# Kernel optimization log

Measured on AMD Instinct MI355X. Metric: run time of the kernel, lower is better.

## Reference

```python
import jax, jax.numpy as jnp
import numpy as np

B, H, W = 1, 48, 160
CIN, CF, D = 1024, 64, 48  # input_features, PSM_features, depth_channel = max_disp/downsample
EPS = 1e-5


def setup_inputs() -> dict:
    key = jax.random.key(0)
    ks = jax.random.split(key, 12)
    z = lambda s: jnp.zeros(s, jnp.float32)
    o = lambda s: jnp.ones(s, jnp.float32)
    return {
        "left_features": jax.random.normal(ks[0], (B, CIN, H, W), jnp.float32),
        "right_features": jax.random.normal(ks[1], (B, CIN, H, W), jnp.float32),
        "conv1_w": jax.random.normal(ks[2], (CF, CIN), jnp.float32) * 0.03,
        "conv1_b": z((CF,)),
        "bn1_g": o((CF,)), "bn1_b": z((CF,)),
        "bn1_m": jax.random.normal(ks[3], (CF,), jnp.float32) * 0.1,
        "bn1_v": jax.random.uniform(ks[4], (CF,), jnp.float32) + 0.5,
        "c3a_w": jax.random.normal(ks[5], (CF, 2 * CF, 3, 3, 3), jnp.float32) * 0.02,
        "c3a_b": z((CF,)),
        "bn3a_g": o((CF,)), "bn3a_b": z((CF,)),
        "bn3a_m": jax.random.normal(ks[6], (CF,), jnp.float32) * 0.1,
        "bn3a_v": jax.random.uniform(ks[7], (CF,), jnp.float32) + 0.5,
        "c3b_w": jax.random.normal(ks[8], (CF, CF, 3, 3, 3), jnp.float32) * 0.02,
        "c3b_b": z((CF,)),
        "bn3b_g": o((CF,)), "bn3b_b": z((CF,)),
        "bn3b_m": jax.random.normal(ks[9], (CF,), jnp.float32) * 0.1,
        "bn3b_v": jax.random.uniform(ks[10], (CF,), jnp.float32) + 0.5,
    }


def _bn(x, g, b, m, v, nsp):
    # eval-mode batchnorm; nsp = number of trailing spatial dims
    sh = (-1,) + (1,) * nsp
    return (x - m.reshape(sh)) * (g.reshape(sh) * jax.lax.rsqrt(v.reshape(sh) + EPS)) + b.reshape(sh)


def reference(left_features, right_features, conv1_w, conv1_b, bn1_g, bn1_b, bn1_m, bn1_v,
              c3a_w, c3a_b, bn3a_g, bn3a_b, bn3a_m, bn3a_v,
              c3b_w, c3b_b, bn3b_g, bn3b_b, bn3b_m, bn3b_v):
    def down(x):
        y = jnp.einsum('oi,bihw->bohw', conv1_w, x) + conv1_b[:, None, None]
        return jax.nn.relu(_bn(y, bn1_g, bn1_b, bn1_m, bn1_v, 2))

    L = down(left_features)   # [B,CF,H,W]
    R = down(right_features)  # [B,CF,H,W]

    # Vectorized shifted cost volume (replaces the Python loop over disparities).
    # For disparity d, output width j: left -> L[...,j] if j>=d else 0; right -> R[...,j-d] if j>=d else 0.
    idx = jnp.arange(W)[None, :] - jnp.arange(D)[:, None]       # [D,W]
    mask = (idx >= 0).astype(L.dtype)                           # [D,W]
    left_vol = L[:, :, :, None, :] * mask                       # [B,CF,H,D,W]
    right_vol = R[:, :, :, jnp.clip(idx, 0, W - 1)] * mask      # [B,CF,H,D,W]
    cost = jnp.concatenate([left_vol, right_vol], axis=1)       # [B,2CF,H,D,W]
    cost = jnp.transpose(cost, (0, 1, 3, 2, 4))                 # [B,2CF,D,H,W]

    def conv3(x, wk, bias):
        y = jax.lax.conv_general_dilated(x, wk, (1, 1, 1), [(1, 1)] * 3,
                                         dimension_numbers=('NCDHW', 'OIDHW', 'NCDHW'))
        return y + bias[:, None, None, None]

    y = jax.nn.relu(_bn(conv3(cost, c3a_w, c3a_b), bn3a_g, bn3a_b, bn3a_m, bn3a_v, 3))
    y = jax.nn.relu(_bn(conv3(y, c3b_w, c3b_b), bn3b_g, bn3b_b, bn3b_m, bn3b_v, 3))
    return y.reshape(B, -1, H, W)  # [B, CF*D, H, W]
```

## Files before the change

kernel.cpp:

```cpp
#include <hip/hip_runtime.h>
#include <hip/hip_bf16.h>


#define HH   48
#define WW   160
#define DDEP 48
#define CIN  1024
#define NPX  (HH*WW)
#define KSPL 8

typedef unsigned short u16;
typedef unsigned int   u32;
typedef __attribute__((ext_vector_type(8))) short bf16x8;
typedef __attribute__((ext_vector_type(4))) float f32x4;
typedef __attribute__((ext_vector_type(4))) u32   u32x4;
typedef __attribute__((ext_vector_type(2))) u32   u32x2;

__device__ __forceinline__ u16 f2bf(float f) {
    u32 u = __builtin_bit_cast(u32, f);
    u32 r = u + 0x7FFFu + ((u >> 16) & 1u);
    return (u16)(r >> 16);
}

__global__ __launch_bounds__(256) void k_prep(
    const float* __restrict__ c3a, const float* __restrict__ c3b,
    const float* __restrict__ cb3a, const float* __restrict__ g3a,
    const float* __restrict__ b3a,  const float* __restrict__ m3a,
    const float* __restrict__ v3a,
    const float* __restrict__ cb3b, const float* __restrict__ g3b,
    const float* __restrict__ b3b,  const float* __restrict__ m3b,
    const float* __restrict__ v3b,
    u16* __restrict__ wa, u16* __restrict__ wb, float* __restrict__ bnc)
{
    int tid = blockIdx.x*256 + threadIdx.x;
    if (tid < 221184) {
        int i = tid & 127, o = (tid >> 7) & 63, tap = tid >> 13;
        wa[tid] = f2bf(c3a[(o*128 + i)*27 + tap]);
    } else {
        int t2 = tid - 221184;
        if (t2 < 110592) {
            int i = t2 & 63;
            int kw = (t2 >> 6) % 3;
            int rest = t2 / 192;
            int o = rest & 63, kdkh = rest >> 6;
            wb[t2] = f2bf(c3b[(o*64 + i)*27 + (kdkh/3)*9 + (kdkh%3)*3 + kw]);
        }
    }
    if (tid < 64) {
        float s = g3a[tid] * rsqrtf(v3a[tid] + 1e-5f);
        bnc[tid]      = s;
        bnc[64 + tid] = (cb3a[tid] - m3a[tid])*s + b3a[tid];
    } else if (tid < 128) {
        int o = tid - 64;
        float s = g3b[o] * rsqrtf(v3b[o] + 1e-5f);
        bnc[128 + o] = s;
        bnc[192 + o] = (cb3b[o] - m3b[o])*s + b3b[o];
    }
}

__global__ __launch_bounds__(256) void k_conv1(
    const float* __restrict__ left, const float* __restrict__ right,
    const float* __restrict__ w1, float* __restrict__ P)
{
    const int img = blockIdx.y;
    const int s   = blockIdx.z;
    const float* x = img ? right : left;
    const int px = blockIdx.x*64 + (threadIdx.x & 63);
    const int o0 = (threadIdx.x >> 6)*16;

    float acc[16];
    #pragma unroll
    for (int oo = 0; oo < 16; ++oo) acc[oo] = 0.f;

    const int ibase = s*(CIN/KSPL);
    for (int it = 0; it < CIN/KSPL; it += 4) {
        const int i = ibase + it;
        float x0 = x[(i+0)*NPX + px];
        float x1 = x[(i+1)*NPX + px];
        float x2 = x[(i+2)*NPX + px];
        float x3 = x[(i+3)*NPX + px];
        #pragma unroll
        for (int oo = 0; oo < 16; ++oo) {
            const float4 wv4 = *(const float4*)(w1 + (size_t)(o0+oo)*CIN + i);
            acc[oo] = fmaf(wv4.w, x3, fmaf(wv4.z, x2,
                      fmaf(wv4.y, x1, fmaf(wv4.x, x0, acc[oo]))));
        }
    }
    float* dst = P + ((size_t)(s*2 + img)*NPX + px)*64 + o0;
    #pragma unroll
    for (int q = 0; q < 4; ++q)
        *(f32x4*)(dst + q*4) = *(const f32x4*)(acc + q*4);
}

__global__ __launch_bounds__(256) void k_conv1_reduce(
    const float* __restrict__ P,
    const float* __restrict__ b1,
    const float* __restrict__ g,  const float* __restrict__ bb,
    const float* __restrict__ m,  const float* __restrict__ v,
    u16* __restrict__ LRb)
{
    const int tid = blockIdx.x*256 + threadIdx.x;
    const int f = tid*4;
    f32x4 acc = *(const f32x4*)(P + f);
    #pragma unroll
    for (int s = 1; s < KSPL; ++s)
        acc += *(const f32x4*)(P + (size_t)(s*2)*(NPX*64) + f);
    const int o0 = f & 63;
    u16 res[4];
    #pragma unroll
    for (int r = 0; r < 4; ++r) {
        int o = o0 + r;
        float sc = g[o] * rsqrtf(v[o] + 1e-5f);
        float val = (acc[r] + b1[o] - m[o])*sc + bb[o];
        res[r] = f2bf(val > 0.f ? val : 0.f);
    }
    *(u32x2*)(LRb + f) = *(const u32x2*)res;
}

__global__ __launch_bounds__(256) void k_conv3a(
    const u16* __restrict__ LRb, const u16* __restrict__ wa,
    const float* __restrict__ bnc, u16* __restrict__ yt)
{
    __shared__ u16 sm[31744];
    u16* Lt = sm;
    u16* Rt = sm + 11520;
    u16* Aw = sm + 23040;

    const int h  = blockIdx.x;
    const int d0 = blockIdx.y*2;
    const int tid = threadIdx.x;
    const int l  = tid & 63;
    const int wv = tid >> 6;
    const int dd = wv >> 1;
    const int wbase = (wv & 1)*80;
    const int l15 = l & 15, l4 = l >> 4;
    const int wcol = wbase + l15;
    const bf16x8 bzero = {0,0,0,0,0,0,0,0};

    f32x4 acc[4][5];
    #pragma unroll
    for (int a = 0; a < 4; ++a)
        #pragma unroll
        for (int b = 0; b < 5; ++b)
            acc[a][b] = (f32x4){0.f,0.f,0.f,0.f};

    for (int kh = 0; kh < 3; ++kh) {
        int hp = h + kh - 1;
        if (hp < 0 || hp >= HH) continue;
        __syncthreads();
        {
            const u16* ls = LRb + (size_t)hp*WW*64;
            const u16* rs = LRb + (size_t)(NPX + hp*WW)*64;
            #pragma unroll
            for (int gq = 0; gq < 5; ++gq) {
                int eb = (gq*256 + tid)*8;
                int wwi = eb >> 6, ii = eb & 63;
                u32x4 va = *(const u32x4*)(ls + eb);
                u32x4 vb = *(const u32x4*)(rs + eb);
                *(u32x4*)(Lt + wwi*72 + ii) = va;
                *(u32x4*)(Rt + wwi*72 + ii) = vb;
            }
        }
        for (int kd = 0; kd < 3; ++kd) {
            int dp = d0 + dd + kd - 1;
            bool dok = (dp >= 0) && (dp < DDEP);
            for (int kw = 0; kw < 3; ++kw) {
                __syncthreads();
                {
                    const u16* as = wa + (size_t)(kd*9 + kh*3 + kw)*8192;
                    #pragma unroll
                    for (int gq = 0; gq < 4; ++gq) {
                        int eb = (gq*256 + tid)*8;
                        int o = eb >> 7, ii = eb & 127;
                        *(u32x4*)(Aw + o*136 + ii) = *(const u32x4*)(as + eb);
                    }
                }
                __syncthreads();

                int laddr[5], raddr[5];
                bool val[5];
                #pragma unroll
                for (int nf = 0; nf < 5; ++nf) {
                    int wp = wcol + nf*16 + kw - 1;
                    bool vv = dok && (wp >= 0) && (wp < WW) && (wp >= dp);
                    val[nf]   = vv;
                    laddr[nf] = (vv ? wp : 0)*72;
                    raddr[nf] = (vv ? (wp - dp) : 0)*72;
                }
                #pragma unroll
                for (int ic = 0; ic < 4; ++ic) {
                    const int kcolA = ic*32 + 8*l4;
                    bf16x8 a0 = *(const bf16x8*)(Aw + ( 0 + l15)*136 + kcolA);
                    bf16x8 a1 = *(const bf16x8*)(Aw + (16 + l15)*136 + kcolA);
                    bf16x8 a2 = *(const bf16x8*)(Aw + (32 + l15)*136 + kcolA);
                    bf16x8 a3 = *(const bf16x8*)(Aw + (48 + l15)*136 + kcolA);
                    const int kin = (ic & 1)*32 + 8*l4;
                    #pragma unroll
                    for (int nf = 0; nf < 5; ++nf) {
                        const u16* bp = (ic < 2) ? (Lt + laddr[nf] + kin)
                                                 : (Rt + raddr[nf] + kin);
                        bf16x8 b = *(const bf16x8*)bp;
                        b = val[nf] ? b : bzero;
                        acc[0][nf] = __builtin_amdgcn_mfma_f32_16x16x32_bf16(a0, b, acc[0][nf], 0, 0, 0);
                        acc[1][nf] = __builtin_amdgcn_mfma_f32_16x16x32_bf16(a1, b, acc[1][nf], 0, 0, 0);
                        acc[2][nf] = __builtin_amdgcn_mfma_f32_16x16x32_bf16(a2, b, acc[2][nf], 0, 0, 0);
                        acc[3][nf] = __builtin_amdgcn_mfma_f32_16x16x32_bf16(a3, b, acc[3][nf], 0, 0, 0);
                    }
                }
            }
        }
    }

    __syncthreads();
    u16* eps = sm + wv*5280;
    float sc[4][4], sh[4][4];
    #pragma unroll
    for (int mf = 0; mf < 4; ++mf)
        #pragma unroll
        for (int r = 0; r < 4; ++r) {
            int o = mf*16 + 4*l4 + r;
            sc[mf][r] = bnc[o];
            sh[mf][r] = bnc[64 + o];
        }
    #pragma unroll
    for (int mf = 0; mf < 4; ++mf)
        #pragma unroll
        for (int nf = 0; nf < 5; ++nf)
            #pragma unroll
            for (int r = 0; r < 4; ++r) {
                float vv = acc[mf][nf][r]*sc[mf][r] + sh[mf][r];
                vv = vv > 0.f ? vv : 0.f;
                eps[(nf*16 + l15)*66 + mf*16 + 4*l4 + r] = f2bf(vv);
            }
    const int dy = d0 + dd;
    u16* yb2 = yt + ((size_t)(dy*HH + h)*8)*1280;
    #pragma unroll
    for (int k = 0; k < 40; ++k) {
        int flat = k*64 + l;
        int c   = flat / 320;
        int rem = flat - c*320;
        int w   = rem >> 2;
        int pr  = (rem & 3)*2;
        u32 vv = *(const u32*)(eps + w*66 + c*8 + pr);
        *(u32*)(yb2 + (size_t)c*1280 + (wbase + w)*8 + pr) = vv;
    }
}

__global__ __launch_bounds__(256) void k_conv3b(
    const u16* __restrict__ yt, const u16* __restrict__ wb,
    const float* __restrict__ bnc, float* __restrict__ outp)
{
    __shared__ u16 A2[12800];

    const int h  = blockIdx.x;
    const int d0 = blockIdx.y*2;
    const int tid = threadIdx.x;
    const int l  = tid & 63;
    const int wv = tid >> 6;
    const int dd = wv >> 1;
    const int wbase = (wv & 1)*80;
    const int l15 = l & 15, l4 = l >> 4;
    const int wcol = wbase + l15;
    const bf16x8 bzero = {0,0,0,0,0,0,0,0};

    f32x4 acc[4][5];
    #pragma unroll
    for (int a = 0; a < 4; ++a)
        #pragma unroll
        for (int b = 0; b < 5; ++b)
            acc[a][b] = (f32x4){0.f,0.f,0.f,0.f};

    for (int kh = 0; kh < 3; ++kh) {
        int hp = h + kh - 1;
        if (hp < 0 || hp >= HH) continue;
        for (int kd = 0; kd < 3; ++kd) {
            __syncthreads();
            {
                const u16* as = wb + (size_t)(kd*3 + kh)*12288;
                #pragma unroll
                for (int q = 0; q < 6; ++q) {
                    int idx = q*256 + tid;
                    int o = idx/24;
                    int cc = (idx - o*24)*8;
                    *(u32x4*)(A2 + o*200 + cc) = *(const u32x4*)(as + (size_t)idx*8);
                }
            }
            __syncthreads();

            const int dpw = d0 + dd + kd - 1;
            const bool dok = (dpw >= 0) && (dpw < DDEP);
            const int dc = min(max(dpw, 0), DDEP-1);
            const u16* yrow = yt + ((size_t)((dc*HH + hp)*8) + l4)*1280;
            for (int kw = 0; kw < 3; ++kw) {
                int gofs[5]; bool val[5];
                #pragma unroll
                for (int nf = 0; nf < 5; ++nf) {
                    int wp = wcol + nf*16 + kw - 1;
                    bool vv = dok && (wp >= 0) && (wp < WW);
                    val[nf]  = vv;
                    gofs[nf] = (vv ? wp : 0)*8;
                }
                #pragma unroll
                for (int ic = 0; ic < 2; ++ic) {
                    const int kcolA = kw*64 + ic*32 + 8*l4;
                    bf16x8 a0 = *(const bf16x8*)(A2 + ( 0 + l15)*200 + kcolA);
                    bf16x8 a1 = *(const bf16x8*)(A2 + (16 + l15)*200 + kcolA);
                    bf16x8 a2 = *(const bf16x8*)(A2 + (32 + l15)*200 + kcolA);
                    bf16x8 a3 = *(const bf16x8*)(A2 + (48 + l15)*200 + kcolA);
                    const u16* yc = yrow + ic*5120;
                    #pragma unroll
                    for (int nf = 0; nf < 5; ++nf) {
                        bf16x8 b = *(const bf16x8*)(yc + gofs[nf]);
                        b = val[nf] ? b : bzero;
                        acc[0][nf] = __builtin_amdgcn_mfma_f32_16x16x32_bf16(a0, b, acc[0][nf], 0, 0, 0);
                        acc[1][nf] = __builtin_amdgcn_mfma_f32_16x16x32_bf16(a1, b, acc[1][nf], 0, 0, 0);
                        acc[2][nf] = __builtin_amdgcn_mfma_f32_16x16x32_bf16(a2, b, acc[2][nf], 0, 0, 0);
                        acc[3][nf] = __builtin_amdgcn_mfma_f32_16x16x32_bf16(a3, b, acc[3][nf], 0, 0, 0);
                    }
                }
            }
        }
    }

    const int dout = d0 + dd;
    #pragma unroll
    for (int mf = 0; mf < 4; ++mf)
        #pragma unroll
        for (int r = 0; r < 4; ++r) {
            int o = mf*16 + 4*l4 + r;
            float s = bnc[128 + o], t = bnc[192 + o];
            size_t base = ((size_t)(o*DDEP + dout)*HH + h)*WW + wbase;
            #pragma unroll
            for (int nf = 0; nf < 5; ++nf) {
                float vv = acc[mf][nf][r]*s + t;
                outp[base + nf*16 + l15] = vv > 0.f ? vv : 0.f;
            }
        }
}

extern "C" void kernel_launch(void* const* d_in, const int* in_sizes, int n_in,
                              void* d_out, int out_size, void* d_ws, size_t ws_size,
                              hipStream_t stream)
{
    const float* left  = (const float*)d_in[0];
    const float* right = (const float*)d_in[1];
    const float* w1    = (const float*)d_in[2];
    const float* b1    = (const float*)d_in[3];
    const float* g1    = (const float*)d_in[4];
    const float* bb1   = (const float*)d_in[5];
    const float* m1    = (const float*)d_in[6];
    const float* v1    = (const float*)d_in[7];
    const float* c3a   = (const float*)d_in[8];
    const float* cb3a  = (const float*)d_in[9];
    const float* g3a   = (const float*)d_in[10];
    const float* b3a   = (const float*)d_in[11];
    const float* m3a   = (const float*)d_in[12];
    const float* v3a   = (const float*)d_in[13];
    const float* c3b   = (const float*)d_in[14];
    const float* cb3b  = (const float*)d_in[15];
    const float* g3b   = (const float*)d_in[16];
    const float* b3b   = (const float*)d_in[17];
    const float* m3b   = (const float*)d_in[18];
    const float* v3b   = (const float*)d_in[19];

    char* ws = (char*)d_ws;
    u16*   LRb = (u16*)ws;
    u16*   wa  = (u16*)(ws + 1966080);
    u16*   wb  = (u16*)(ws + 1966080 + 442368);
    float* bnc = (float*)(ws + 1966080 + 442368 + 221184);
    u16*   yt  = (u16*)(ws + 1966080 + 442368 + 221184 + 1024);
    if (ws_size < 49816576) return;

    float* P = (float*)d_out;

    k_prep<<<dim3(1296), dim3(256), 0, stream>>>(
        c3a, c3b, cb3a, g3a, b3a, m3a, v3a, cb3b, g3b, b3b, m3b, v3b, wa, wb, bnc);
    k_conv1<<<dim3(120, 2, KSPL), dim3(256), 0, stream>>>(
        left, right, w1, P);
    k_conv1_reduce<<<dim3(960), dim3(256), 0, stream>>>(
        P, b1, g1, bb1, m1, v1, LRb);
    k_conv3a<<<dim3(48, 24), dim3(256), 0, stream>>>(LRb, wa, bnc, yt);
    k_conv3b<<<dim3(48, 24), dim3(256), 0, stream>>>(yt, wb, bnc, (float*)d_out);
}
```

Measured before the change: 389.7 us.

## Stage conv1 weights in LDS and read conv3a inputs directly in channel-blocked layout

Conv1 now loads its slice of the weight matrix into shared memory once per block, so the inner loop no longer re-reads weights from global memory. The conv1 reduce writes the downsampled features in a channel-blocked [img][h][c/8][w][8] layout. Conv3a then reads its B operands straight from global memory in that layout instead of staging left and right rows through LDS, and writes its outputs directly without the LDS epilogue transpose. This frees LDS and removes barriers, but conv3a now depends on cache hits for repeated global reads, and the stride-1280 pattern may coalesce less well.

After: 358.8 us. -7.9%, faster.

```diff
diff --git a/kernel.cpp b/kernel.cpp
--- a/kernel.cpp
+++ b/kernel.cpp
@@ -62,17 +62,28 @@
     const float* __restrict__ left, const float* __restrict__ right,
     const float* __restrict__ w1, float* __restrict__ P)
 {
+    __shared__ float Ws[8192];
     const int img = blockIdx.y;
     const int s   = blockIdx.z;
     const float* x = img ? right : left;
-    const int px = blockIdx.x*64 + (threadIdx.x & 63);
-    const int o0 = (threadIdx.x >> 6)*16;
+    const int tid = threadIdx.x;
+    const int px = blockIdx.x*64 + (tid & 63);
+    const int o0 = (tid >> 6)*16;
+    const int ibase = s*(CIN/KSPL);
+
+    #pragma unroll
+    for (int q = 0; q < 8; ++q) {
+        int idx = q*256 + tid;
+        int o = idx >> 5, ii = (idx & 31)*4;
+        *(f32x4*)(Ws + o*128 + ii) =
+            *(const f32x4*)(w1 + (size_t)o*CIN + ibase + ii);
+    }
+    __syncthreads();
 
     float acc[16];
     #pragma unroll
     for (int oo = 0; oo < 16; ++oo) acc[oo] = 0.f;
 
-    const int ibase = s*(CIN/KSPL);
     for (int it = 0; it < CIN/KSPL; it += 4) {
         const int i = ibase + it;
         float x0 = x[(i+0)*NPX + px];
@@ -81,7 +92,7 @@
         float x3 = x[(i+3)*NPX + px];
         #pragma unroll
         for (int oo = 0; oo < 16; ++oo) {
-            const float4 wv4 = *(const float4*)(w1 + (size_t)(o0+oo)*CIN + i);
+            const float4 wv4 = *(const float4*)(Ws + (o0+oo)*128 + it);
             acc[oo] = fmaf(wv4.w, x3, fmaf(wv4.z, x2,
                       fmaf(wv4.y, x1, fmaf(wv4.x, x0, acc[oo]))));
         }
@@ -106,6 +117,9 @@
     for (int s = 1; s < KSPL; ++s)
         acc += *(const f32x4*)(P + (size_t)(s*2)*(NPX*64) + f);
     const int o0 = f & 63;
+    const int px = f >> 6;
+    const int img = px / NPX, pxl = px - img*NPX;
+    const int h = pxl / WW, w = pxl - h*WW;
     u16 res[4];
     #pragma unroll
     for (int r = 0; r < 4; ++r) {
@@ -114,17 +128,16 @@
         float val = (acc[r] + b1[o] - m[o])*sc + bb[o];
         res[r] = f2bf(val > 0.f ? val : 0.f);
     }
-    *(u32x2*)(LRb + f) = *(const u32x2*)res;
+    u16* dst = LRb + (size_t)img*491520 + h*10240 + (o0 >> 3)*1280
+                   + w*8 + (o0 & 7);
+    *(u32x2*)dst = *(const u32x2*)res;
 }
 
 __global__ __launch_bounds__(256) void k_conv3a(
     const u16* __restrict__ LRb, const u16* __restrict__ wa,
     const float* __restrict__ bnc, u16* __restrict__ yt)
 {
-    __shared__ u16 sm[31744];
-    u16* Lt = sm;
-    u16* Rt = sm + 11520;
-    u16* Aw = sm + 23040;
+    __shared__ u16 Aw[8704];
 
     const int h  = blockIdx.x;
     const int d0 = blockIdx.y*2;
@@ -147,23 +160,11 @@
     for (int kh = 0; kh < 3; ++kh) {
         int hp = h + kh - 1;
         if (hp < 0 || hp >= HH) continue;
-        __syncthreads();
-        {
-            const u16* ls = LRb + (size_t)hp*WW*64;
-            const u16* rs = LRb + (size_t)(NPX + hp*WW)*64;
-            #pragma unroll
-            for (int gq = 0; gq < 5; ++gq) {
-                int eb = (gq*256 + tid)*8;
-                int wwi = eb >> 6, ii = eb & 63;
-                u32x4 va = *(const u32x4*)(ls + eb);
-                u32x4 vb = *(const u32x4*)(rs + eb);
-                *(u32x4*)(Lt + wwi*72 + ii) = va;
-                *(u32x4*)(Rt + wwi*72 + ii) = vb;
-            }
-        }
+        const u16* lrow = LRb + (size_t)hp*10240;
+        const u16* rrow = LRb + 491520 + (size_t)hp*10240;
         for (int kd = 0; kd < 3; ++kd) {
-            int dp = d0 + dd + kd - 1;
-            bool dok = (dp >= 0) && (dp < DDEP);
+            const int dp = d0 + dd + kd - 1;
+            const bool dok = (dp >= 0) && (dp < DDEP);
             for (int kw = 0; kw < 3; ++kw) {
                 __syncthreads();
                 {
@@ -177,15 +178,15 @@
                 }
                 __syncthreads();
 
-                int laddr[5], raddr[5];
+                int lofs[5], rofs[5];
                 bool val[5];
                 #pragma unroll
                 for (int nf = 0; nf < 5; ++nf) {
                     int wp = wcol + nf*16 + kw - 1;
                     bool vv = dok && (wp >= 0) && (wp < WW) && (wp >= dp);
-                    val[nf]   = vv;
-                    laddr[nf] = (vv ? wp : 0)*72;
-                    raddr[nf] = (vv ? (wp - dp) : 0)*72;
+                    val[nf]  = vv;
+                    lofs[nf] = (vv ? wp : 0)*8;
+                    rofs[nf] = (vv ? (wp - dp) : 0)*8;
                 }
                 #pragma unroll
                 for (int ic = 0; ic < 4; ++ic) {
@@ -194,12 +195,12 @@
                     bf16x8 a1 = *(const bf16x8*)(Aw + (16 + l15)*136 + kcolA);
                     bf16x8 a2 = *(const bf16x8*)(Aw + (32 + l15)*136 + kcolA);
                     bf16x8 a3 = *(const bf16x8*)(Aw + (48 + l15)*136 + kcolA);
-                    const int kin = (ic & 1)*32 + 8*l4;
+                    const u16* bbase = ((ic < 2) ? lrow : rrow)
+                                     + (size_t)((ic & 1)*4 + l4)*1280;
                     #pragma unroll
                     for (int nf = 0; nf < 5; ++nf) {
-                        const u16* bp = (ic < 2) ? (Lt + laddr[nf] + kin)
-                                                 : (Rt + raddr[nf] + kin);
-                        bf16x8 b = *(const bf16x8*)bp;
+                        bf16x8 b = *(const bf16x8*)(bbase +
+                                       ((ic < 2) ? lofs[nf] : rofs[nf]));
                         b = val[nf] ? b : bzero;
                         acc[0][nf] = __builtin_amdgcn_mfma_f32_16x16x32_bf16(a0, b, acc[0][nf], 0, 0, 0);
                         acc[1][nf] = __builtin_amdgcn_mfma_f32_16x16x32_bf16(a1, b, acc[1][nf], 0, 0, 0);
@@ -211,8 +212,6 @@
         }
     }
 
-    __syncthreads();
-    u16* eps = sm + wv*5280;
     float sc[4][4], sh[4][4];
     #pragma unroll
     for (int mf = 0; mf < 4; ++mf)
@@ -222,28 +221,24 @@
             sc[mf][r] = bnc[o];
             sh[mf][r] = bnc[64 + o];
         }
+    const int dy = d0 + dd;
+    u16* rowb = yt + (size_t)(dy*HH + h)*10240;
     #pragma unroll
     for (int mf = 0; mf < 4; ++mf)
         #pragma unroll
-        for (int nf = 0; nf < 5; ++nf)
+        for (int nf = 0; nf < 5; ++nf) {
+            const int w = wbase + nf*16 + l15;
             #pragma unroll
-            for (int r = 0; r < 4; ++r) {
-                float vv = acc[mf][nf][r]*sc[mf][r] + sh[mf][r];
-                vv = vv > 0.f ? vv : 0.f;
-                eps[(nf*16 + l15)*66 + mf*16 + 4*l4 + r] = f2bf(vv);
-            }
-    const int dy = d0 + dd;
-    u16* yb2 = yt + ((size_t)(dy*HH + h)*8)*1280;
-    #pragma unroll
-    for (int k = 0; k < 40; ++k) {
-        int flat = k*64 + l;
-        int c   = flat / 320;
-        int rem = flat - c*320;
-        int w   = rem >> 2;
-        int pr  = (rem & 3)*2;
-        u32 vv = *(const u32*)(eps + w*66 + c*8 + pr);
-        *(u32*)(yb2 + (size_t)c*1280 + (wbase + w)*8 + pr) = vv;
-    }
+            for (int rp = 0; rp < 2; ++rp) {
+                int o_lo = mf*16 + 4*l4 + rp*2;
+                float v0 = acc[mf][nf][rp*2]  *sc[mf][rp*2]   + sh[mf][rp*2];
+                float v1 = acc[mf][nf][rp*2+1]*sc[mf][rp*2+1] + sh[mf][rp*2+1];
+                v0 = v0 > 0.f ? v0 : 0.f;
+                v1 = v1 > 0.f ? v1 : 0.f;
+                u32 pk = (u32)f2bf(v0) | ((u32)f2bf(v1) << 16);
+                *(u32*)(rowb + (o_lo >> 3)*1280 + w*8 + (o_lo & 7)) = pk;
+            }
+        }
 }
 
 __global__ __launch_bounds__(256) void k_conv3b(
```

## Stage conv1 weights in shared memory, raise K-split, and retile the LR layout

Applied to the files above, without the earlier changes.

The conv1 kernel now loads its 64x64 weight slice into shared memory once per block instead of reading the weights from global memory inside the inner loop. The K-split doubles from 8 to 16, so there are more blocks but each does a shorter reduction. The reduce kernel writes bf16 L/R features in a channel-chunked [img][h][c/8][w][8] layout, and conv3a reads that layout for its tile loads. The tradeoffs are a larger partial-sum buffer and more work in the reduce pass; the layout change could also affect coalescing.

Result: faster. 320.5 us (-17.8%).

```diff
diff --git a/kernel.cpp b/kernel.cpp
--- a/kernel.cpp
+++ b/kernel.cpp
@@ -7,7 +7,7 @@
 #define DDEP 48
 #define CIN  1024
 #define NPX  (HH*WW)
-#define KSPL 8
+#define KSPL 16
 
 typedef unsigned short u16;
 typedef unsigned int   u32;
@@ -62,17 +62,28 @@
     const float* __restrict__ left, const float* __restrict__ right,
     const float* __restrict__ w1, float* __restrict__ P)
 {
+    __shared__ float Ws[4096];
     const int img = blockIdx.y;
     const int s   = blockIdx.z;
     const float* x = img ? right : left;
-    const int px = blockIdx.x*64 + (threadIdx.x & 63);
-    const int o0 = (threadIdx.x >> 6)*16;
+    const int tid = threadIdx.x;
+    const int px = blockIdx.x*64 + (tid & 63);
+    const int o0 = (tid >> 6)*16;
+    const int ibase = s*(CIN/KSPL);
+
+    #pragma unroll
+    for (int q = 0; q < 4; ++q) {
+        int idx = q*256 + tid;
+        int o = idx >> 4, ii = (idx & 15)*4;
+        *(f32x4*)(Ws + o*64 + ii) =
+            *(const f32x4*)(w1 + (size_t)o*CIN + ibase + ii);
+    }
+    __syncthreads();
 
     float acc[16];
     #pragma unroll
     for (int oo = 0; oo < 16; ++oo) acc[oo] = 0.f;
 
-    const int ibase = s*(CIN/KSPL);
     for (int it = 0; it < CIN/KSPL; it += 4) {
         const int i = ibase + it;
         float x0 = x[(i+0)*NPX + px];
@@ -81,7 +92,7 @@
         float x3 = x[(i+3)*NPX + px];
         #pragma unroll
         for (int oo = 0; oo < 16; ++oo) {
-            const float4 wv4 = *(const float4*)(w1 + (size_t)(o0+oo)*CIN + i);
+            const float4 wv4 = *(const float4*)(Ws + (o0+oo)*64 + it);
             acc[oo] = fmaf(wv4.w, x3, fmaf(wv4.z, x2,
                       fmaf(wv4.y, x1, fmaf(wv4.x, x0, acc[oo]))));
         }
@@ -106,6 +117,9 @@
     for (int s = 1; s < KSPL; ++s)
         acc += *(const f32x4*)(P + (size_t)(s*2)*(NPX*64) + f);
     const int o0 = f & 63;
+    const int px = f >> 6;
+    const int img = px / NPX, pxl = px - img*NPX;
+    const int h = pxl / WW, w = pxl - h*WW;
     u16 res[4];
     #pragma unroll
     for (int r = 0; r < 4; ++r) {
@@ -114,7 +128,9 @@
         float val = (acc[r] + b1[o] - m[o])*sc + bb[o];
         res[r] = f2bf(val > 0.f ? val : 0.f);
     }
-    *(u32x2*)(LRb + f) = *(const u32x2*)res;
+    u16* dst = LRb + (size_t)img*491520 + h*10240 + (o0 >> 3)*1280
+                   + w*8 + (o0 & 7);
+    *(u32x2*)dst = *(const u32x2*)res;
 }
 
 __global__ __launch_bounds__(256) void k_conv3a(
@@ -149,16 +165,17 @@
         if (hp < 0 || hp >= HH) continue;
         __syncthreads();
         {
-            const u16* ls = LRb + (size_t)hp*WW*64;
-            const u16* rs = LRb + (size_t)(NPX + hp*WW)*64;
+            const u16* ls = LRb + (size_t)hp*10240;
+            const u16* rs = LRb + 491520 + (size_t)hp*10240;
             #pragma unroll
             for (int gq = 0; gq < 5; ++gq) {
                 int eb = (gq*256 + tid)*8;
-                int wwi = eb >> 6, ii = eb & 63;
+                int c = eb / 1280, rem = eb - c*1280;
+                int w = rem >> 3;
                 u32x4 va = *(const u32x4*)(ls + eb);
                 u32x4 vb = *(const u32x4*)(rs + eb);
-                *(u32x4*)(Lt + wwi*72 + ii) = va;
-                *(u32x4*)(Rt + wwi*72 + ii) = vb;
+                *(u32x4*)(Lt + w*72 + c*8) = va;
+                *(u32x4*)(Rt + w*72 + c*8) = vb;
             }
         }
         for (int kd = 0; kd < 3; ++kd) {
@@ -233,7 +250,7 @@
                 eps[(nf*16 + l15)*66 + mf*16 + 4*l4 + r] = f2bf(vv);
             }
     const int dy = d0 + dd;
-    u16* yb2 = yt + ((size_t)(dy*HH + h)*8)*1280;
+    u16* yb2 = yt + ((size_t)(dy*HH + h))*10240;
     #pragma unroll
     for (int k = 0; k < 40; ++k) {
         int flat = k*64 + l;
```
